# Performance work log

Hardware: AMD Instinct MI355X
Metric: run time of the kernel (lower is better)

## Reference

```python
import jax, jax.numpy as jnp
import numpy as np

N0, N1, N2, N3 = 40000, 10000, 2500, 625
C_IN, C_HID = 64, 256
E0 = N0 * 6
KS = (6, 7, 8)  # KnnEdges(start_k=6, k_increment=1): k = 6 + level
DEPTH = 3


def gcn_conv(x, edge_index, W, b):
    n = x.shape[0]
    loop = jnp.arange(n, dtype=edge_index.dtype)
    src = jnp.concatenate([edge_index[0], loop])
    dst = jnp.concatenate([edge_index[1], loop])
    deg = jax.ops.segment_sum(jnp.ones(src.shape[0], x.dtype), dst, num_segments=n)
    inv = jax.lax.rsqrt(jnp.maximum(deg, 1e-12))
    norm = (inv[src] * inv[dst])[:, None]
    h = x @ W
    return jax.ops.segment_sum(h[src] * norm, dst, num_segments=n) + b


def knn_edges(pos, k):
    # dynamic KNN graph on pooled positions (single graph -> no batch masking)
    n = pos.shape[0]
    sq = jnp.sum(pos * pos, axis=-1)
    d = sq[:, None] + sq[None, :] - 2.0 * (pos @ pos.T)  # [n, n] squared dists
    d = d.at[jnp.arange(n), jnp.arange(n)].set(jnp.inf)  # exclude self
    idx = jax.lax.top_k(-d, k)[1]                        # [n, k] neighbor ids
    src = idx.reshape(-1).astype(jnp.int32)
    dst = jnp.repeat(jnp.arange(n, dtype=jnp.int32), k)
    return jnp.stack([src, dst])


def setup_inputs():
    key = jax.random.key(0)
    ks = jax.random.split(key, 16)
    x = jax.random.normal(ks[0], (N0, C_IN), jnp.float32)
    pos = jax.random.uniform(ks[1], (N0, 2), dtype=jnp.float32)
    edge_index = jax.random.randint(ks[2], (2, E0), 0, N0, jnp.int32)
    # random pooling = randperm prefix (data-independent, precomputed)
    perm1 = jax.random.permutation(ks[3], N0)[:N1].astype(jnp.int32)
    perm2 = jax.random.permutation(ks[4], N1)[:N2].astype(jnp.int32)
    perm3 = jax.random.permutation(ks[5], N2)[:N3].astype(jnp.int32)

    def w(k, i, o):
        return jax.random.normal(k, (i, o), jnp.float32) * (1.0 / np.sqrt(i))

    zb = lambda: jnp.zeros((C_HID,), jnp.float32)
    return dict(
        x=x, pos=pos, edge_index=edge_index,
        perm1=perm1, perm2=perm2, perm3=perm3,
        Wd0=w(ks[6], C_IN, C_HID), bd0=zb(),
        Wd1=w(ks[7], C_HID, C_HID), bd1=zb(),
        Wd2=w(ks[8], C_HID, C_HID), bd2=zb(),
        Wu0=w(ks[9], C_HID, C_HID), bu0=zb(),
        Wu1=w(ks[10], C_HID, C_HID), bu1=zb(),
        Wu2=w(ks[11], C_HID, C_HID), bu2=zb(),
        Wlin=w(ks[12], C_HID, C_HID), blin=zb(),
    )


def reference(x, pos, edge_index, perm1, perm2, perm3,
              Wd0, bd0, Wd1, bd1, Wd2, bd2,
              Wu0, bu0, Wu1, bu1, Wu2, bu2, Wlin, blin):
    down_W, down_b = (Wd0, Wd1, Wd2), (bd0, bd1, bd2)
    up_W, up_b = (Wu0, Wu1, Wu2), (bu0, bu1, bu2)
    perms = (perm1, perm2, perm3)
    edge_indices = [edge_index]
    n_levels = [x.shape[0]]
    # encoder: conv -> relu -> random pool -> dynamic KNN rebuild
    for i in range(DEPTH):
        x = jax.nn.relu(gcn_conv(x, edge_indices[-1], down_W[i], down_b[i]))
        pos = pos[perms[i]]
        edge_indices.append(knn_edges(pos, KS[i]))
        x = x[perms[i]]
        n_levels.append(x.shape[0])
    # decoder: scatter unpool (up[perm] = x) -> conv -> relu
    for i in range(DEPTH):
        up = jnp.zeros((n_levels[-i - 2], x.shape[1]), x.dtype).at[perms[-i - 1]].set(x)
        x = jax.nn.relu(gcn_conv(up, edge_indices[-i - 2], up_W[i], up_b[i]))
    return x @ Wlin + blin
```

## Files before the change

### kernel.cpp

```cpp
#include <hip/hip_runtime.h>
#include <hip/hip_bf16.h>

#define N0 40000
#define N1 10000
#define N2 2500
#define N3 625
#define E0 240000
#define CIN 64
#define CH 256
#define NBLK ((N0 + 255) / 256)

__global__ void count_deg(const int* __restrict__ dst, int* __restrict__ deg, int e) {
    int i = blockIdx.x * blockDim.x + threadIdx.x;
    if (i < e) atomicAdd(&deg[dst[i]], 1);
}

__global__ __launch_bounds__(256) void scan_blocks(const int* __restrict__ deg,
                                                   int* __restrict__ incl,
                                                   int* __restrict__ bsum, int n) {
    __shared__ int s[256];
    int i = blockIdx.x * 256 + threadIdx.x;
    s[threadIdx.x] = (i < n) ? deg[i] : 0;
    __syncthreads();
#pragma unroll
    for (int off = 1; off < 256; off <<= 1) {
        int t = (threadIdx.x >= off) ? s[threadIdx.x - off] : 0;
        __syncthreads();
        s[threadIdx.x] += t;
        __syncthreads();
    }
    if (i < n) incl[i] = s[threadIdx.x];
    if (threadIdx.x == 255) bsum[blockIdx.x] = s[255];
}

__global__ __launch_bounds__(256) void scan_bsums(int* __restrict__ bsum, int nb) {
    __shared__ int s[256];
    s[threadIdx.x] = (threadIdx.x < nb) ? bsum[threadIdx.x] : 0;
    __syncthreads();
#pragma unroll
    for (int off = 1; off < 256; off <<= 1) {
        int t = (threadIdx.x >= off) ? s[threadIdx.x - off] : 0;
        __syncthreads();
        s[threadIdx.x] += t;
        __syncthreads();
    }
    if (threadIdx.x < nb) bsum[threadIdx.x] = s[threadIdx.x];
}

__global__ void finalize_rowptr(const int* __restrict__ incl, const int* __restrict__ bsum,
                                int* __restrict__ rowptr, int n) {
    int i = blockIdx.x * blockDim.x + threadIdx.x;
    if (i == 0) rowptr[0] = 0;
    if (i < n) {
        int b = i >> 8;
        int off = b ? bsum[b - 1] : 0;
        rowptr[i + 1] = incl[i] + off;
    }
}

__global__ void copy_int(const int* __restrict__ a, int* __restrict__ b, int n) {
    int i = blockIdx.x * blockDim.x + threadIdx.x;
    if (i < n) b[i] = a[i];
}
__global__ void fill_csr(const int* __restrict__ src, const int* __restrict__ dst,
                         int* __restrict__ cursor, int* __restrict__ colsrc, int e) {
    int i = blockIdx.x * blockDim.x + threadIdx.x;
    if (i < e) {
        int d = dst[i];
        int p = atomicAdd(&cursor[d], 1);
        colsrc[p] = src[i];
    }
}
__global__ void make_inv(const int* __restrict__ deg, double* __restrict__ inv, int n) {
    int i = blockIdx.x * blockDim.x + threadIdx.x;
    if (i < n) inv[i] = 1.0 / sqrt((double)(deg[i] + 1));
}

__global__ __launch_bounds__(256) void gemm_f32(
    const float* __restrict__ A, const int* __restrict__ gidx,
    const float* __restrict__ W, const float* __restrict__ bias,
    float* __restrict__ out, int M, int K)
{
    __shared__ float As[16][68];
    __shared__ float Bs[16][68];
    const int tid = threadIdx.x;
    const int tx = tid & 15, ty = tid >> 4;
    const int row0 = blockIdx.x * 64, col0 = blockIdx.y * 64;
    const int sr = tid >> 2;
    const int skq = (tid & 3) * 4;
    const int bkk = tid >> 4;
    const int bc4 = (tid & 15) * 4;
    const int arow = row0 + sr;
    const bool rowok = arow < M;
    long arr = 0;
    if (rowok) arr = (long)(gidx ? gidx[arow] : arow) * K;

    float acc[4][4] = {};
    for (int k0 = 0; k0 < K; k0 += 16) {
        float4 av = make_float4(0.f, 0.f, 0.f, 0.f);
        if (rowok) av = *reinterpret_cast<const float4*>(&A[arr + k0 + skq]);
        As[skq + 0][sr] = av.x;
        As[skq + 1][sr] = av.y;
        As[skq + 2][sr] = av.z;
        As[skq + 3][sr] = av.w;
        float4 bv = *reinterpret_cast<const float4*>(&W[(long)(k0 + bkk) * CH + col0 + bc4]);
        *reinterpret_cast<float4*>(&Bs[bkk][bc4]) = bv;
        __syncthreads();
#pragma unroll
        for (int kk = 0; kk < 16; ++kk) {
            float4 a4 = *reinterpret_cast<const float4*>(&As[kk][ty * 4]);
            float4 b4 = *reinterpret_cast<const float4*>(&Bs[kk][tx * 4]);
            float a[4] = {a4.x, a4.y, a4.z, a4.w};
            float b[4] = {b4.x, b4.y, b4.z, b4.w};
#pragma unroll
            for (int i = 0; i < 4; i++)
#pragma unroll
                for (int j = 0; j < 4; j++) acc[i][j] += a[i] * b[j];
        }
        __syncthreads();
    }
#pragma unroll
    for (int i = 0; i < 4; i++) {
        int row = row0 + ty * 4 + i;
        if (row >= M) continue;
#pragma unroll
        for (int j = 0; j < 4; j++) {
            int col = col0 + tx * 4 + j;
            float v = acc[i][j];
            if (bias) v += bias[col];
            out[(long)row * CH + col] = v;
        }
    }
}

__global__ __launch_bounds__(256) void agg_e0(
    const float* __restrict__ h, const int* __restrict__ rowptr,
    const int* __restrict__ colsrc, const double* __restrict__ inv,
    const float* __restrict__ bias, float* __restrict__ out, int n)
{
    __shared__ int s_src[256];
    __shared__ double s_nrm[256];
    int i = blockIdx.x, c = threadIdx.x;
    int r0 = rowptr[i], r1 = rowptr[i + 1];
    double invd = inv[i];
    double acc = (double)h[(long)i * CH + c] * (invd * invd);
    for (int base = r0; base < r1; base += 256) {
        int m = min(256, r1 - base);
        __syncthreads();
        if (c < m) {
            int s = colsrc[base + c];
            s_src[c] = s;
            s_nrm[c] = invd * inv[s];
        }
        __syncthreads();
        for (int j = 0; j < m; ++j)
            acc += (double)h[(long)s_src[j] * CH + c] * s_nrm[j];
    }
    double v = acc + (double)bias[c];
    out[(long)i * CH + c] = (float)fmax(v, 0.0);
}

__global__ void agg_knn(const float* __restrict__ h, const int* __restrict__ idx,
                        const float* __restrict__ b, float* __restrict__ out,
                        int n, int k, double s) {
    int i = blockIdx.x, c = threadIdx.x;
    double acc = (double)h[(long)i * CH + c];
    for (int j = 0; j < k; ++j) {
        int nb = idx[i * k + j];
        acc += (double)h[(long)nb * CH + c];
    }
    double v = acc * s + (double)b[c];
    out[(long)i * CH + c] = (float)fmax(v, 0.0);
}

template <int K>
__global__ __launch_bounds__(64) void knn_kernel(const float* __restrict__ pos, int n,
                                                 int* __restrict__ outIdx) {
    const float INF = __int_as_float(0x7f800000);
    int q = blockIdx.x;
    int lane = threadIdx.x;
    const float2* p2 = (const float2*)pos;
    const float4* p4 = (const float4*)pos;
    float2 qp = p2[q];
    float sqq = __fmaf_rn(qp.y, qp.y, __fmul_rn(qp.x, qp.x));
    float bd[K];
    int bi[K];
#pragma unroll
    for (int t = 0; t < K; ++t) { bd[t] = INF; bi[t] = 0x7fffffff; }
    for (int jj = lane * 2; jj < n; jj += 128) {
        float4 pp = p4[jj >> 1];
#pragma unroll
        for (int c = 0; c < 2; ++c) {
            int j = jj + c;
            float px = c ? pp.z : pp.x;
            float py = c ? pp.w : pp.y;
            float sqj = __fmaf_rn(py, py, __fmul_rn(px, px));
            float dot = __fmaf_rn(qp.y, py, __fmul_rn(qp.x, px));
            float t1  = __fadd_rn(sqq, sqj);
            float d   = __fmaf_rn(-2.0f, dot, t1);
            d = (j == q) ? INF : d;
            if (d < bd[K - 1]) {
                bd[K - 1] = d; bi[K - 1] = j;
#pragma unroll
                for (int t = K - 1; t > 0; --t) {
                    if (bd[t] < bd[t - 1]) {
                        float td = bd[t]; bd[t] = bd[t - 1]; bd[t - 1] = td;
                        int ti = bi[t]; bi[t] = bi[t - 1]; bi[t - 1] = ti;
                    }
                }
            }
        }
    }
    for (int r = 0; r < K; ++r) {
        float md = bd[0];
        int mi = bi[0];
#pragma unroll
        for (int off = 32; off; off >>= 1) {
            float od = __shfl_xor(md, off, 64);
            int oi = __shfl_xor(mi, off, 64);
            if (od < md || (od == md && oi < mi)) { md = od; mi = oi; }
        }
        if (md == bd[0] && mi == bi[0]) {
#pragma unroll
            for (int t = 0; t < K - 1; ++t) { bd[t] = bd[t + 1]; bi[t] = bi[t + 1]; }
            bd[K - 1] = INF; bi[K - 1] = 0x7fffffff;
        }
        if (lane == 0) outIdx[q * K + r] = mi;
    }
}

__global__ void gather_pos(const float* __restrict__ pos, const int* __restrict__ perm,
                           float* __restrict__ out, int m) {
    int i = blockIdx.x * blockDim.x + threadIdx.x;
    if (i < m) {
        int p = perm[i];
        ((float2*)out)[i] = ((const float2*)pos)[p];
    }
}
__global__ void copy_rows(const float* __restrict__ srcb, const int* __restrict__ perm,
                          float* __restrict__ dst, int m) {
    int i = blockIdx.x, c = threadIdx.x;
    int r = perm[i];
    dst[(long)r * CH + c] = srcb[(long)r * CH + c];
}
__global__ void scatter_rows(const float* __restrict__ srcb, const int* __restrict__ perm,
                             float* __restrict__ dst, int m) {
    int i = blockIdx.x, c = threadIdx.x;
    dst[(long)perm[i] * CH + c] = srcb[(long)i * CH + c];
}

extern "C" void kernel_launch(void* const* d_in, const int* in_sizes, int n_in,
                              void* d_out, int out_size, void* d_ws, size_t ws_size,
                              hipStream_t stream) {
    const float* x    = (const float*)d_in[0];
    const float* pos  = (const float*)d_in[1];
    const int*   ei   = (const int*)d_in[2];
    const int*   perm1 = (const int*)d_in[3];
    const int*   perm2 = (const int*)d_in[4];
    const int*   perm3 = (const int*)d_in[5];
    const float* Wd0 = (const float*)d_in[6],  *bd0 = (const float*)d_in[7];
    const float* Wd1 = (const float*)d_in[8],  *bd1 = (const float*)d_in[9];
    const float* Wd2 = (const float*)d_in[10], *bd2 = (const float*)d_in[11];
    const float* Wu0 = (const float*)d_in[12], *bu0 = (const float*)d_in[13];
    const float* Wu1 = (const float*)d_in[14], *bu1 = (const float*)d_in[15];
    const float* Wu2 = (const float*)d_in[16], *bu2 = (const float*)d_in[17];
    const float* Wlin = (const float*)d_in[18], *blin = (const float*)d_in[19];
    float* out = (float*)d_out;

    double* inv0 = (double*)d_ws;
    float* pos1 = (float*)(inv0 + N0);
    float* pos2 = pos1 + N1 * 2;
    float* A   = pos2 + N2 * 2;
    float* C_  = A + (long)N0 * CH;
    float* D_  = C_ + (long)N1 * CH;
    int* degI   = (int*)(D_ + (long)N1 * CH);
    int* rowptr = degI + N0;
    int* cursor = rowptr + N0 + 1;
    int* colsrc = cursor + N0;
    int* idx1   = colsrc + E0;
    int* idx2   = idx1 + N1 * 6;
    int* incl   = idx2 + N2 * 7;
    int* bsum   = incl + N0;
    float* B = out;

    const int* e_src = ei;
    const int* e_dst = ei + E0;

    hipMemsetAsync(degI, 0, (size_t)N0 * sizeof(int), stream);
    count_deg<<<(E0 + 255) / 256, 256, 0, stream>>>(e_dst, degI, E0);
    scan_blocks<<<NBLK, 256, 0, stream>>>(degI, incl, bsum, N0);
    scan_bsums<<<1, 256, 0, stream>>>(bsum, NBLK);
    finalize_rowptr<<<(N0 + 255) / 256, 256, 0, stream>>>(incl, bsum, rowptr, N0);
    copy_int<<<(N0 + 255) / 256, 256, 0, stream>>>(rowptr, cursor, N0);
    fill_csr<<<(E0 + 255) / 256, 256, 0, stream>>>(e_src, e_dst, cursor, colsrc, E0);
    make_inv<<<(N0 + 255) / 256, 256, 0, stream>>>(degI, inv0, N0);

    gemm_f32<<<dim3((N0 + 63) / 64, 4), 256, 0, stream>>>(x, nullptr, Wd0, nullptr, A, N0, CIN);
    agg_e0<<<N0, 256, 0, stream>>>(A, rowptr, colsrc, inv0, bd0, B, N0);

    gather_pos<<<(N1 + 255) / 256, 256, 0, stream>>>(pos, perm1, pos1, N1);
    knn_kernel<6><<<N1, 64, 0, stream>>>(pos1, N1, idx1);

    gemm_f32<<<dim3((N1 + 63) / 64, 4), 256, 0, stream>>>(B, perm1, Wd1, nullptr, C_, N1, CH);
    agg_knn<<<N1, 256, 0, stream>>>(C_, idx1, bd1, D_, N1, 6, 1.0 / 7.0);

    gather_pos<<<(N2 + 255) / 256, 256, 0, stream>>>(pos1, perm2, pos2, N2);
    knn_kernel<7><<<N2, 64, 0, stream>>>(pos2, N2, idx2);

    gemm_f32<<<dim3((N2 + 63) / 64, 4), 256, 0, stream>>>(D_, perm2, Wd2, nullptr, C_, N2, CH);
    agg_knn<<<N2, 256, 0, stream>>>(C_, idx2, bd2, D_, N2, 7, 1.0 / 8.0);

    hipMemsetAsync(C_, 0, (size_t)N2 * CH * sizeof(float), stream);
    copy_rows<<<N3, 256, 0, stream>>>(D_, perm3, C_, N3);
    gemm_f32<<<dim3((N2 + 63) / 64, 4), 256, 0, stream>>>(C_, nullptr, Wu0, nullptr, D_, N2, CH);
    agg_knn<<<N2, 256, 0, stream>>>(D_, idx2, bu0, C_, N2, 7, 1.0 / 8.0);

    hipMemsetAsync(D_, 0, (size_t)N1 * CH * sizeof(float), stream);
    scatter_rows<<<N2, 256, 0, stream>>>(C_, perm2, D_, N2);
    gemm_f32<<<dim3((N1 + 63) / 64, 4), 256, 0, stream>>>(D_, nullptr, Wu1, nullptr, C_, N1, CH);
    agg_knn<<<N1, 256, 0, stream>>>(C_, idx1, bu1, D_, N1, 6, 1.0 / 7.0);

    hipMemsetAsync(A, 0, (size_t)N0 * CH * sizeof(float), stream);
    scatter_rows<<<N1, 256, 0, stream>>>(D_, perm1, A, N1);
    gemm_f32<<<dim3((N0 + 63) / 64, 4), 256, 0, stream>>>(A, nullptr, Wu2, nullptr, B, N0, CH);
    agg_e0<<<N0, 256, 0, stream>>>(B, rowptr, colsrc, inv0, bu2, A, N0);

    gemm_f32<<<dim3((N0 + 63) / 64, 4), 256, 0, stream>>>(A, nullptr, Wlin, blin, out, N0, CH);
}
```

Baseline: 641.0 us.

## Enlarge GEMM tiles to 128x128 and prune KNN candidates with a wave-wide threshold

The fp32 GEMM now computes a 128x128 output tile per block, with a 2x2 set of 4x4 micro-tiles per thread and vectorised float4 stores and bias loads. This cuts shared-memory traffic and global loads per FLOP but raises register use and halves the number of blocks. The KNN kernel also keeps a threshold equal to the wave-wide minimum of each lane's Kth-best distance, updated with shuffles each iteration, so lanes skip insertions that cannot reach the global top-K. This trades extra shuffle reductions per iteration for fewer sorted-insert operations.

```diff
diff --git a/kernel.cpp b/kernel.cpp
--- a/kernel.cpp
+++ b/kernel.cpp
@@ -81,56 +81,74 @@
     const float* __restrict__ W, const float* __restrict__ bias,
     float* __restrict__ out, int M, int K)
 {
-    __shared__ float As[16][68];
-    __shared__ float Bs[16][68];
+    __shared__ float As[16][132];
+    __shared__ float Bs[16][132];
     const int tid = threadIdx.x;
     const int tx = tid & 15, ty = tid >> 4;
-    const int row0 = blockIdx.x * 64, col0 = blockIdx.y * 64;
+    const int row0 = blockIdx.x * 128, col0 = blockIdx.y * 128;
     const int sr = tid >> 2;
     const int skq = (tid & 3) * 4;
-    const int bkk = tid >> 4;
-    const int bc4 = (tid & 15) * 4;
-    const int arow = row0 + sr;
-    const bool rowok = arow < M;
-    long arr = 0;
-    if (rowok) arr = (long)(gidx ? gidx[arow] : arow) * K;
-
-    float acc[4][4] = {};
+    const int ar0 = row0 + sr, ar1 = row0 + 64 + sr;
+    const bool ok0 = ar0 < M, ok1 = ar1 < M;
+    long g0 = 0, g1 = 0;
+    if (ok0) g0 = (long)(gidx ? gidx[ar0] : ar0) * K;
+    if (ok1) g1 = (long)(gidx ? gidx[ar1] : ar1) * K;
+    const int bkk = tid >> 5;
+    const int bc4 = (tid & 31) * 4;
+
+    float acc[2][2][4][4] = {};
     for (int k0 = 0; k0 < K; k0 += 16) {
-        float4 av = make_float4(0.f, 0.f, 0.f, 0.f);
-        if (rowok) av = *reinterpret_cast<const float4*>(&A[arr + k0 + skq]);
-        As[skq + 0][sr] = av.x;
-        As[skq + 1][sr] = av.y;
-        As[skq + 2][sr] = av.z;
-        As[skq + 3][sr] = av.w;
-        float4 bv = *reinterpret_cast<const float4*>(&W[(long)(k0 + bkk) * CH + col0 + bc4]);
-        *reinterpret_cast<float4*>(&Bs[bkk][bc4]) = bv;
+        float4 av0 = make_float4(0.f, 0.f, 0.f, 0.f);
+        float4 av1 = make_float4(0.f, 0.f, 0.f, 0.f);
+        if (ok0) av0 = *reinterpret_cast<const float4*>(&A[g0 + k0 + skq]);
+        if (ok1) av1 = *reinterpret_cast<const float4*>(&A[g1 + k0 + skq]);
+        float4 bv0 = *reinterpret_cast<const float4*>(&W[(long)(k0 + bkk) * CH + col0 + bc4]);
+        float4 bv1 = *reinterpret_cast<const float4*>(&W[(long)(k0 + bkk + 8) * CH + col0 + bc4]);
+        As[skq + 0][sr] = av0.x;  As[skq + 1][sr] = av0.y;
+        As[skq + 2][sr] = av0.z;  As[skq + 3][sr] = av0.w;
+        As[skq + 0][64 + sr] = av1.x;  As[skq + 1][64 + sr] = av1.y;
+        As[skq + 2][64 + sr] = av1.z;  As[skq + 3][64 + sr] = av1.w;
+        *reinterpret_cast<float4*>(&Bs[bkk][bc4]) = bv0;
+        *reinterpret_cast<float4*>(&Bs[bkk + 8][bc4]) = bv1;
         __syncthreads();
 #pragma unroll
         for (int kk = 0; kk < 16; ++kk) {
-            float4 a4 = *reinterpret_cast<const float4*>(&As[kk][ty * 4]);
-            float4 b4 = *reinterpret_cast<const float4*>(&Bs[kk][tx * 4]);
-            float a[4] = {a4.x, a4.y, a4.z, a4.w};
-            float b[4] = {b4.x, b4.y, b4.z, b4.w};
-#pragma unroll
-            for (int i = 0; i < 4; i++)
-#pragma unroll
-                for (int j = 0; j < 4; j++) acc[i][j] += a[i] * b[j];
-        }
-        __syncthreads();
-    }
-#pragma unroll
-    for (int i = 0; i < 4; i++) {
-        int row = row0 + ty * 4 + i;
-        if (row >= M) continue;
-#pragma unroll
-        for (int j = 0; j < 4; j++) {
-            int col = col0 + tx * 4 + j;
-            float v = acc[i][j];
-            if (bias) v += bias[col];
-            out[(long)row * CH + col] = v;
-        }
-    }
+            float4 a0 = *reinterpret_cast<const float4*>(&As[kk][ty * 4]);
+            float4 a1 = *reinterpret_cast<const float4*>(&As[kk][64 + ty * 4]);
+            float4 b0 = *reinterpret_cast<const float4*>(&Bs[kk][tx * 4]);
+            float4 b1 = *reinterpret_cast<const float4*>(&Bs[kk][64 + tx * 4]);
+            float ar[2][4] = {{a0.x, a0.y, a0.z, a0.w}, {a1.x, a1.y, a1.z, a1.w}};
+            float br[2][4] = {{b0.x, b0.y, b0.z, b0.w}, {b1.x, b1.y, b1.z, b1.w}};
+#pragma unroll
+            for (int rh = 0; rh < 2; ++rh)
+#pragma unroll
+                for (int ch = 0; ch < 2; ++ch)
+#pragma unroll
+                    for (int i = 0; i < 4; ++i)
+#pragma unroll
+                        for (int j = 0; j < 4; ++j)
+                            acc[rh][ch][i][j] += ar[rh][i] * br[ch][j];
+        }
+        __syncthreads();
+    }
+#pragma unroll
+    for (int rh = 0; rh < 2; ++rh)
+#pragma unroll
+        for (int i = 0; i < 4; ++i) {
+            int row = row0 + rh * 64 + ty * 4 + i;
+            if (row >= M) continue;
+#pragma unroll
+            for (int ch = 0; ch < 2; ++ch) {
+                int col = col0 + ch * 64 + tx * 4;
+                float4 v = make_float4(acc[rh][ch][i][0], acc[rh][ch][i][1],
+                                       acc[rh][ch][i][2], acc[rh][ch][i][3]);
+                if (bias) {
+                    float4 bv = *reinterpret_cast<const float4*>(&bias[col]);
+                    v.x += bv.x; v.y += bv.y; v.z += bv.z; v.w += bv.w;
+                }
+                *reinterpret_cast<float4*>(&out[(long)row * CH + col]) = v;
+            }
+        }
 }
 
 __global__ __launch_bounds__(256) void agg_e0(
@@ -187,6 +205,7 @@
     int bi[K];
 #pragma unroll
     for (int t = 0; t < K; ++t) { bd[t] = INF; bi[t] = 0x7fffffff; }
+    float thrG = INF;
     for (int jj = lane * 2; jj < n; jj += 128) {
         float4 pp = p4[jj >> 1];
 #pragma unroll
@@ -199,7 +218,7 @@
             float t1  = __fadd_rn(sqq, sqj);
             float d   = __fmaf_rn(-2.0f, dot, t1);
             d = (j == q) ? INF : d;
-            if (d < bd[K - 1]) {
+            if (d < bd[K - 1] && d <= thrG) {
                 bd[K - 1] = d; bi[K - 1] = j;
 #pragma unroll
                 for (int t = K - 1; t > 0; --t) {
@@ -210,6 +229,13 @@
                 }
             }
         }
+        float m = bd[K - 1];
+#pragma unroll
+        for (int off = 32; off; off >>= 1) {
+            float o = __shfl_xor(m, off, 64);
+            m = o < m ? o : m;
+        }
+        thrG = m;
     }
     for (int r = 0; r < K; ++r) {
         float md = bd[0];
@@ -295,35 +321,35 @@
     fill_csr<<<(E0 + 255) / 256, 256, 0, stream>>>(e_src, e_dst, cursor, colsrc, E0);
     make_inv<<<(N0 + 255) / 256, 256, 0, stream>>>(degI, inv0, N0);
 
-    gemm_f32<<<dim3((N0 + 63) / 64, 4), 256, 0, stream>>>(x, nullptr, Wd0, nullptr, A, N0, CIN);
+    gemm_f32<<<dim3((N0 + 127) / 128, 2), 256, 0, stream>>>(x, nullptr, Wd0, nullptr, A, N0, CIN);
     agg_e0<<<N0, 256, 0, stream>>>(A, rowptr, colsrc, inv0, bd0, B, N0);
 
     gather_pos<<<(N1 + 255) / 256, 256, 0, stream>>>(pos, perm1, pos1, N1);
     knn_kernel<6><<<N1, 64, 0, stream>>>(pos1, N1, idx1);
 
-    gemm_f32<<<dim3((N1 + 63) / 64, 4), 256, 0, stream>>>(B, perm1, Wd1, nullptr, C_, N1, CH);
+    gemm_f32<<<dim3((N1 + 127) / 128, 2), 256, 0, stream>>>(B, perm1, Wd1, nullptr, C_, N1, CH);
     agg_knn<<<N1, 256, 0, stream>>>(C_, idx1, bd1, D_, N1, 6, 1.0 / 7.0);
 
     gather_pos<<<(N2 + 255) / 256, 256, 0, stream>>>(pos1, perm2, pos2, N2);
     knn_kernel<7><<<N2, 64, 0, stream>>>(pos2, N2, idx2);
 
-    gemm_f32<<<dim3((N2 + 63) / 64, 4), 256, 0, stream>>>(D_, perm2, Wd2, nullptr, C_, N2, CH);
+    gemm_f32<<<dim3((N2 + 127) / 128, 2), 256, 0, stream>>>(D_, perm2, Wd2, nullptr, C_, N2, CH);
     agg_knn<<<N2, 256, 0, stream>>>(C_, idx2, bd2, D_, N2, 7, 1.0 / 8.0);
 
     hipMemsetAsync(C_, 0, (size_t)N2 * CH * sizeof(float), stream);
     copy_rows<<<N3, 256, 0, stream>>>(D_, perm3, C_, N3);
-    gemm_f32<<<dim3((N2 + 63) / 64, 4), 256, 0, stream>>>(C_, nullptr, Wu0, nullptr, D_, N2, CH);
+    gemm_f32<<<dim3((N2 + 127) / 128, 2), 256, 0, stream>>>(C_, nullptr, Wu0, nullptr, D_, N2, CH);
     agg_knn<<<N2, 256, 0, stream>>>(D_, idx2, bu0, C_, N2, 7, 1.0 / 8.0);
 
     hipMemsetAsync(D_, 0, (size_t)N1 * CH * sizeof(float), stream);
     scatter_rows<<<N2, 256, 0, stream>>>(C_, perm2, D_, N2);
-    gemm_f32<<<dim3((N1 + 63) / 64, 4), 256, 0, stream>>>(D_, nullptr, Wu1, nullptr, C_, N1, CH);
+    gemm_f32<<<dim3((N1 + 127) / 128, 2), 256, 0, stream>>>(D_, nullptr, Wu1, nullptr, C_, N1, CH);
     agg_knn<<<N1, 256, 0, stream>>>(C_, idx1, bu1, D_, N1, 6, 1.0 / 7.0);
 
     hipMemsetAsync(A, 0, (size_t)N0 * CH * sizeof(float), stream);
     scatter_rows<<<N1, 256, 0, stream>>>(D_, perm1, A, N1);
-    gemm_f32<<<dim3((N0 + 63) / 64, 4), 256, 0, stream>>>(A, nullptr, Wu2, nullptr, B, N0, CH);
+    gemm_f32<<<dim3((N0 + 127) / 128, 2), 256, 0, stream>>>(A, nullptr, Wu2, nullptr, B, N0, CH);
     agg_e0<<<N0, 256, 0, stream>>>(B, rowptr, colsrc, inv0, bu2, A, N0);
 
-    gemm_f32<<<dim3((N0 + 63) / 64, 4), 256, 0, stream>>>(A, nullptr, Wlin, blin, out, N0, CH);
-}
+    gemm_f32<<<dim3((N0 + 127) / 128, 2), 256, 0, stream>>>(A, nullptr, Wlin, blin, out, N0, CH);
+}
```

Result: slower. 731.6 us (+14.1%).

## Restructure KNN as thread-per-query over LDS candidate chunks with merge pass

Applied to the files above, without the earlier changes.

Replaces the block-per-query KNN (64 lanes scanning all points, then K rounds of wave shuffle reductions) with one thread per query. Each block stages a chunk of candidate positions in LDS, keeps a private top-K, and writes partial results to a scratch buffer. A second kernel merges the chunk partials per query. This is meant to remove the repeated global position reads and the per-query shuffle reductions, at the cost of an extra launch and scratch traffic. Tie-breaking still follows the ascending index order of the original.

```diff
diff --git a/kernel.cpp b/kernel.cpp
--- a/kernel.cpp
+++ b/kernel.cpp
@@ -174,33 +174,72 @@
 }
 
 template <int K>
-__global__ __launch_bounds__(64) void knn_kernel(const float* __restrict__ pos, int n,
-                                                 int* __restrict__ outIdx) {
+__global__ __launch_bounds__(64) void knn_partial(const float* __restrict__ pos, int n, int csz,
+                                                  float2* __restrict__ part) {
+    extern __shared__ float2 lpos[];
     const float INF = __int_as_float(0x7f800000);
-    int q = blockIdx.x;
     int lane = threadIdx.x;
+    int q = blockIdx.x * 64 + lane;
+    int ct = blockIdx.y;
+    int c0 = ct * csz;
+    int c1 = min(n, c0 + csz);
+    int m = c1 - c0;
     const float2* p2 = (const float2*)pos;
-    const float4* p4 = (const float4*)pos;
-    float2 qp = p2[q];
+    for (int t = lane; t < m; t += 64) lpos[t] = p2[c0 + t];
+    __syncthreads();
+    int qq = (q < n) ? q : 0;
+    float2 qp = p2[qq];
     float sqq = __fmaf_rn(qp.y, qp.y, __fmul_rn(qp.x, qp.x));
     float bd[K];
     int bi[K];
 #pragma unroll
     for (int t = 0; t < K; ++t) { bd[t] = INF; bi[t] = 0x7fffffff; }
-    for (int jj = lane * 2; jj < n; jj += 128) {
-        float4 pp = p4[jj >> 1];
-#pragma unroll
-        for (int c = 0; c < 2; ++c) {
-            int j = jj + c;
-            float px = c ? pp.z : pp.x;
-            float py = c ? pp.w : pp.y;
-            float sqj = __fmaf_rn(py, py, __fmul_rn(px, px));
-            float dot = __fmaf_rn(qp.y, py, __fmul_rn(qp.x, px));
-            float t1  = __fadd_rn(sqq, sqj);
-            float d   = __fmaf_rn(-2.0f, dot, t1);
-            d = (j == q) ? INF : d;
+#pragma unroll 4
+    for (int jc = 0; jc < m; ++jc) {
+        float2 pj = lpos[jc];
+        int j = c0 + jc;
+        float sqj = __fmaf_rn(pj.y, pj.y, __fmul_rn(pj.x, pj.x));
+        float dot = __fmaf_rn(qp.y, pj.y, __fmul_rn(qp.x, pj.x));
+        float t1  = __fadd_rn(sqq, sqj);
+        float d   = __fmaf_rn(-2.0f, dot, t1);
+        d = (j == q) ? INF : d;
+        if (d < bd[K - 1]) {
+            bd[K - 1] = d; bi[K - 1] = j;
+#pragma unroll
+            for (int t = K - 1; t > 0; --t) {
+                if (bd[t] < bd[t - 1]) {
+                    float td = bd[t]; bd[t] = bd[t - 1]; bd[t - 1] = td;
+                    int ti = bi[t]; bi[t] = bi[t - 1]; bi[t - 1] = ti;
+                }
+            }
+        }
+    }
+    if (q < n) {
+#pragma unroll
+        for (int r = 0; r < K; ++r)
+            part[(ct * K + r) * n + q] = make_float2(bd[r], __int_as_float(bi[r]));
+    }
+}
+
+template <int K, int C>
+__global__ __launch_bounds__(64) void knn_merge(const float2* __restrict__ part, int n,
+                                                int* __restrict__ outIdx) {
+    const float INF = __int_as_float(0x7f800000);
+    int q = blockIdx.x * 64 + threadIdx.x;
+    if (q >= n) return;
+    float bd[K];
+    int bi[K];
+#pragma unroll
+    for (int t = 0; t < K; ++t) { bd[t] = INF; bi[t] = 0x7fffffff; }
+#pragma unroll
+    for (int ct = 0; ct < C; ++ct) {
+#pragma unroll
+        for (int r = 0; r < K; ++r) {
+            float2 p = part[(ct * K + r) * n + q];
+            float d = p.x;
+            int i = __float_as_int(p.y);
             if (d < bd[K - 1]) {
-                bd[K - 1] = d; bi[K - 1] = j;
+                bd[K - 1] = d; bi[K - 1] = i;
 #pragma unroll
                 for (int t = K - 1; t > 0; --t) {
                     if (bd[t] < bd[t - 1]) {
@@ -211,22 +250,8 @@
             }
         }
     }
-    for (int r = 0; r < K; ++r) {
-        float md = bd[0];
-        int mi = bi[0];
-#pragma unroll
-        for (int off = 32; off; off >>= 1) {
-            float od = __shfl_xor(md, off, 64);
-            int oi = __shfl_xor(mi, off, 64);
-            if (od < md || (od == md && oi < mi)) { md = od; mi = oi; }
-        }
-        if (md == bd[0] && mi == bi[0]) {
-#pragma unroll
-            for (int t = 0; t < K - 1; ++t) { bd[t] = bd[t + 1]; bi[t] = bi[t + 1]; }
-            bd[K - 1] = INF; bi[K - 1] = 0x7fffffff;
-        }
-        if (lane == 0) outIdx[q * K + r] = mi;
-    }
+#pragma unroll
+    for (int r = 0; r < K; ++r) outIdx[q * K + r] = bi[r];
 }
 
 __global__ void gather_pos(const float* __restrict__ pos, const int* __restrict__ perm,
@@ -282,6 +307,7 @@
     int* incl   = idx2 + N2 * 7;
     int* bsum   = incl + N0;
     float* B = out;
+    float2* part = (float2*)A;
 
     const int* e_src = ei;
     const int* e_dst = ei + E0;
@@ -299,13 +325,21 @@
     agg_e0<<<N0, 256, 0, stream>>>(A, rowptr, colsrc, inv0, bd0, B, N0);
 
     gather_pos<<<(N1 + 255) / 256, 256, 0, stream>>>(pos, perm1, pos1, N1);
-    knn_kernel<6><<<N1, 64, 0, stream>>>(pos1, N1, idx1);
+    {
+        const int C1 = 8, CSZ1 = (N1 + C1 - 1) / C1;
+        knn_partial<6><<<dim3((N1 + 63) / 64, C1), 64, CSZ1 * sizeof(float2), stream>>>(pos1, N1, CSZ1, part);
+        knn_merge<6, 8><<<(N1 + 63) / 64, 64, 0, stream>>>(part, N1, idx1);
+    }
 
     gemm_f32<<<dim3((N1 + 63) / 64, 4), 256, 0, stream>>>(B, perm1, Wd1, nullptr, C_, N1, CH);
     agg_knn<<<N1, 256, 0, stream>>>(C_, idx1, bd1, D_, N1, 6, 1.0 / 7.0);
 
     gather_pos<<<(N2 + 255) / 256, 256, 0, stream>>>(pos1, perm2, pos2, N2);
-    knn_kernel<7><<<N2, 64, 0, stream>>>(pos2, N2, idx2);
+    {
+        const int C2 = 4, CSZ2 = (N2 + C2 - 1) / C2;
+        knn_partial<7><<<dim3((N2 + 63) / 64, C2), 64, CSZ2 * sizeof(float2), stream>>>(pos2, N2, CSZ2, part);
+        knn_merge<7, 4><<<(N2 + 63) / 64, 64, 0, stream>>>(part, N2, idx2);
+    }
 
     gemm_f32<<<dim3((N2 + 63) / 64, 4), 256, 0, stream>>>(D_, perm2, Wd2, nullptr, C_, N2, CH);
     agg_knn<<<N2, 256, 0, stream>>>(C_, idx2, bd2, D_, N2, 7, 1.0 / 8.0);
```

Measured after the change: 776.4 us. 21.1% more time.

## Replace brute-force KNN with uniform-grid spatial binning and ring search

Applied to the files above, without the earlier changes.

Replaces the all-pairs KNN scan, which used one wavefront per query, with a uniform grid built on the unit square: points are counted into cells, prefix-scanned, and scattered into cell-sorted arrays. Each query thread then searches rings of cells outward until the ring distance exceeds the current k-th best distance. This cuts the O(n^2) distance work down to roughly O(n·k). In exchange it adds several small kernel launches, and it assumes positions lie in [0,1]. Ties are broken by index, and the epsilon-based early exit has to reproduce the brute-force neighbor set exactly.

```diff
diff --git a/kernel.cpp b/kernel.cpp
--- a/kernel.cpp
+++ b/kernel.cpp
@@ -1,5 +1,6 @@
 #include <hip/hip_runtime.h>
 #include <hip/hip_bf16.h>
+#include <stdint.h>
 
 #define N0 40000
 #define N1 10000
@@ -173,60 +174,92 @@
     out[(long)i * CH + c] = (float)fmax(v, 0.0);
 }
 
+__global__ void cell_count(const float* __restrict__ pos, int n, int G, int* __restrict__ cnt) {
+    int i = blockIdx.x * blockDim.x + threadIdx.x;
+    if (i < n) {
+        float2 p = ((const float2*)pos)[i];
+        int cx = min(G - 1, (int)(p.x * G));
+        int cy = min(G - 1, (int)(p.y * G));
+        atomicAdd(&cnt[cy * G + cx], 1);
+    }
+}
+__global__ void cell_fill(const float* __restrict__ pos, int n, int G, int* __restrict__ cur,
+                          float2* __restrict__ cpos, int* __restrict__ cidx) {
+    int i = blockIdx.x * blockDim.x + threadIdx.x;
+    if (i < n) {
+        float2 p = ((const float2*)pos)[i];
+        int cx = min(G - 1, (int)(p.x * G));
+        int cy = min(G - 1, (int)(p.y * G));
+        int t = atomicAdd(&cur[cy * G + cx], 1);
+        cpos[t] = p;
+        cidx[t] = i;
+    }
+}
+
 template <int K>
-__global__ __launch_bounds__(64) void knn_kernel(const float* __restrict__ pos, int n,
-                                                 int* __restrict__ outIdx) {
+__global__ void knn_grid(const float* __restrict__ pos, int n, int G,
+                         const int* __restrict__ cellptr,
+                         const float2* __restrict__ cpos,
+                         const int* __restrict__ cidx,
+                         int* __restrict__ outIdx) {
+    int q = blockIdx.x * blockDim.x + threadIdx.x;
+    if (q >= n) return;
     const float INF = __int_as_float(0x7f800000);
-    int q = blockIdx.x;
-    int lane = threadIdx.x;
-    const float2* p2 = (const float2*)pos;
-    const float4* p4 = (const float4*)pos;
-    float2 qp = p2[q];
+    const float EPS = 1e-5f;
+    float h = 1.0f / (float)G;
+    float2 qp = ((const float2*)pos)[q];
     float sqq = __fmaf_rn(qp.y, qp.y, __fmul_rn(qp.x, qp.x));
+    int cx = min(G - 1, (int)(qp.x * G));
+    int cy = min(G - 1, (int)(qp.y * G));
     float bd[K];
     int bi[K];
 #pragma unroll
     for (int t = 0; t < K; ++t) { bd[t] = INF; bi[t] = 0x7fffffff; }
-    for (int jj = lane * 2; jj < n; jj += 128) {
-        float4 pp = p4[jj >> 1];
-#pragma unroll
-        for (int c = 0; c < 2; ++c) {
-            int j = jj + c;
-            float px = c ? pp.z : pp.x;
-            float py = c ? pp.w : pp.y;
-            float sqj = __fmaf_rn(py, py, __fmul_rn(px, px));
-            float dot = __fmaf_rn(qp.y, py, __fmul_rn(qp.x, px));
+
+    auto visit = [&](int xx, int yy) {
+        int ci = yy * G + xx;
+        int s = cellptr[ci], e = cellptr[ci + 1];
+        for (int t = s; t < e; ++t) {
+            float2 pj = cpos[t];
+            int j = cidx[t];
+            float sqj = __fmaf_rn(pj.y, pj.y, __fmul_rn(pj.x, pj.x));
+            float dot = __fmaf_rn(qp.y, pj.y, __fmul_rn(qp.x, pj.x));
             float t1  = __fadd_rn(sqq, sqj);
             float d   = __fmaf_rn(-2.0f, dot, t1);
-            d = (j == q) ? INF : d;
-            if (d < bd[K - 1]) {
+            if (j == q) continue;
+            if (d < bd[K - 1] || (d == bd[K - 1] && j < bi[K - 1])) {
                 bd[K - 1] = d; bi[K - 1] = j;
 #pragma unroll
-                for (int t = K - 1; t > 0; --t) {
-                    if (bd[t] < bd[t - 1]) {
-                        float td = bd[t]; bd[t] = bd[t - 1]; bd[t - 1] = td;
-                        int ti = bi[t]; bi[t] = bi[t - 1]; bi[t - 1] = ti;
+                for (int t2 = K - 1; t2 > 0; --t2) {
+                    bool sw = (bd[t2] < bd[t2 - 1]) ||
+                              (bd[t2] == bd[t2 - 1] && bi[t2] < bi[t2 - 1]);
+                    if (sw) {
+                        float td = bd[t2]; bd[t2] = bd[t2 - 1]; bd[t2 - 1] = td;
+                        int ti = bi[t2]; bi[t2] = bi[t2 - 1]; bi[t2 - 1] = ti;
                     }
                 }
             }
         }
-    }
-    for (int r = 0; r < K; ++r) {
-        float md = bd[0];
-        int mi = bi[0];
-#pragma unroll
-        for (int off = 32; off; off >>= 1) {
-            float od = __shfl_xor(md, off, 64);
-            int oi = __shfl_xor(mi, off, 64);
-            if (od < md || (od == md && oi < mi)) { md = od; mi = oi; }
-        }
-        if (md == bd[0] && mi == bi[0]) {
-#pragma unroll
-            for (int t = 0; t < K - 1; ++t) { bd[t] = bd[t + 1]; bi[t] = bi[t + 1]; }
-            bd[K - 1] = INF; bi[K - 1] = 0x7fffffff;
-        }
-        if (lane == 0) outIdx[q * K + r] = mi;
-    }
+    };
+
+    for (int c = 0; c < G; ++c) {
+        if (c > 0 && bi[K - 1] != 0x7fffffff) {
+            float lim = (float)(c - 1) * h;
+            if (lim * lim > bd[K - 1] + EPS) break;
+        }
+        int y0 = max(0, cy - c), y1 = min(G - 1, cy + c);
+        for (int yy = y0; yy <= y1; ++yy) {
+            if (yy == cy - c || yy == cy + c) {
+                int x0 = max(0, cx - c), x1 = min(G - 1, cx + c);
+                for (int xx = x0; xx <= x1; ++xx) visit(xx, yy);
+            } else {
+                if (cx - c >= 0) visit(cx - c, yy);
+                if (cx + c <= G - 1) visit(cx + c, yy);
+            }
+        }
+    }
+#pragma unroll
+    for (int r = 0; r < K; ++r) outIdx[q * K + r] = bi[r];
 }
 
 __global__ void gather_pos(const float* __restrict__ pos, const int* __restrict__ perm,
@@ -281,6 +314,11 @@
     int* idx2   = idx1 + N1 * 6;
     int* incl   = idx2 + N2 * 7;
     int* bsum   = incl + N0;
+    int* cellcnt = bsum + NBLK;
+    int* cellptr = cellcnt + 4096;
+    int* ccur    = cellptr + 4097;
+    int* cellidx = ccur + 4096;
+    float2* cellpos = (float2*)(((uintptr_t)(cellidx + N1) + 15) & ~(uintptr_t)15);
     float* B = out;
 
     const int* e_src = ei;
@@ -299,13 +337,33 @@
     agg_e0<<<N0, 256, 0, stream>>>(A, rowptr, colsrc, inv0, bd0, B, N0);
 
     gather_pos<<<(N1 + 255) / 256, 256, 0, stream>>>(pos, perm1, pos1, N1);
-    knn_kernel<6><<<N1, 64, 0, stream>>>(pos1, N1, idx1);
+    {
+        const int G1 = 64, NC1 = G1 * G1;
+        hipMemsetAsync(cellcnt, 0, (size_t)NC1 * sizeof(int), stream);
+        cell_count<<<(N1 + 255) / 256, 256, 0, stream>>>(pos1, N1, G1, cellcnt);
+        scan_blocks<<<NC1 / 256, 256, 0, stream>>>(cellcnt, incl, bsum, NC1);
+        scan_bsums<<<1, 256, 0, stream>>>(bsum, NC1 / 256);
+        finalize_rowptr<<<(NC1 + 255) / 256, 256, 0, stream>>>(incl, bsum, cellptr, NC1);
+        copy_int<<<(NC1 + 255) / 256, 256, 0, stream>>>(cellptr, ccur, NC1);
+        cell_fill<<<(N1 + 255) / 256, 256, 0, stream>>>(pos1, N1, G1, ccur, cellpos, cellidx);
+        knn_grid<6><<<(N1 + 255) / 256, 256, 0, stream>>>(pos1, N1, G1, cellptr, cellpos, cellidx, idx1);
+    }
 
     gemm_f32<<<dim3((N1 + 63) / 64, 4), 256, 0, stream>>>(B, perm1, Wd1, nullptr, C_, N1, CH);
     agg_knn<<<N1, 256, 0, stream>>>(C_, idx1, bd1, D_, N1, 6, 1.0 / 7.0);
 
     gather_pos<<<(N2 + 255) / 256, 256, 0, stream>>>(pos1, perm2, pos2, N2);
-    knn_kernel<7><<<N2, 64, 0, stream>>>(pos2, N2, idx2);
+    {
+        const int G2 = 32, NC2 = G2 * G2;
+        hipMemsetAsync(cellcnt, 0, (size_t)NC2 * sizeof(int), stream);
+        cell_count<<<(N2 + 255) / 256, 256, 0, stream>>>(pos2, N2, G2, cellcnt);
+        scan_blocks<<<NC2 / 256, 256, 0, stream>>>(cellcnt, incl, bsum, NC2);
+        scan_bsums<<<1, 256, 0, stream>>>(bsum, NC2 / 256);
+        finalize_rowptr<<<(NC2 + 255) / 256, 256, 0, stream>>>(incl, bsum, cellptr, NC2);
+        copy_int<<<(NC2 + 255) / 256, 256, 0, stream>>>(cellptr, ccur, NC2);
+        cell_fill<<<(N2 + 255) / 256, 256, 0, stream>>>(pos2, N2, G2, ccur, cellpos, cellidx);
+        knn_grid<7><<<(N2 + 255) / 256, 256, 0, stream>>>(pos2, N2, G2, cellptr, cellpos, cellidx, idx2);
+    }
 
     gemm_f32<<<dim3((N2 + 63) / 64, 4), 256, 0, stream>>>(D_, perm2, Wd2, nullptr, C_, N2, CH);
     agg_knn<<<N2, 256, 0, stream>>>(C_, idx2, bd2, D_, N2, 7, 1.0 / 8.0);
```

Result: slower. 727.2 us (+13.4%).
